# Optimization experiments

Hardware: AMD Instinct MI355X
Metric: run time of the kernel (lower is better)

Reference implementation:

```python
import jax, jax.numpy as jnp
import numpy as np
from jax import lax

BN_EPS = 1e-5

def _conv(x, w, groups=1, pad=0):
    return lax.conv_general_dilated(
        x, w, window_strides=(1, 1), padding=[(pad, pad), (pad, pad)],
        dimension_numbers=('NCHW', 'OIHW', 'NCHW'), feature_group_count=groups)

def _gather2d(imgf, yi, xi, H, W):
    # imgf: [B,C,H*W] flattened image; yi, xi: [B,C,H,W] int32 corner indices
    valid = (yi >= 0) & (yi < H) & (xi >= 0) & (xi < W)
    yc = jnp.clip(yi, 0, H - 1)
    xc = jnp.clip(xi, 0, W - 1)
    idx = (yc * W + xc).reshape(imgf.shape[0], imgf.shape[1], -1)
    v = jnp.take_along_axis(imgf, idx, axis=2).reshape(yi.shape)
    return jnp.where(valid, v, 0.0)

def _bilinear_sample(img, y, x):
    # img: [B,C,H,W]; y, x: [B,C,H,W] float sample coords (zero outside)
    B, C, H, W = img.shape
    imgf = img.reshape(B, C, H * W)
    y0 = jnp.floor(y)
    x0 = jnp.floor(x)
    wy = y - y0  # weight for y1 corner
    wx = x - x0
    y0i = y0.astype(jnp.int32); y1i = y0i + 1
    x0i = x0.astype(jnp.int32); x1i = x0i + 1
    v00 = _gather2d(imgf, y0i, x0i, H, W)
    v01 = _gather2d(imgf, y0i, x1i, H, W)
    v10 = _gather2d(imgf, y1i, x0i, H, W)
    v11 = _gather2d(imgf, y1i, x1i, H, W)
    return ((1 - wy) * (1 - wx) * v00 + (1 - wy) * wx * v01
            + wy * (1 - wx) * v10 + wy * wx * v11)

def setup_inputs() -> dict:
    key = jax.random.key(0)
    ks = jax.random.split(key, 6)
    B, C, OC, H, W = 4, 64, 64, 256, 256
    return {
        'x': jax.random.normal(ks[0], (B, C, H, W), jnp.float32),
        'dw_weight': jax.random.normal(ks[1], (C, 1, 3, 3), jnp.float32) * 0.2,
        'pw_weight': jax.random.normal(ks[2], (3 * C, C, 1, 1), jnp.float32) * 0.1,
        'weight': jax.random.normal(ks[3], (OC, C, 1, 1), jnp.float32) * 0.1,
        'bias': jax.random.normal(ks[4], (OC,), jnp.float32) * 0.1,
        'gamma': jnp.ones((OC,), jnp.float32),
        'beta': jnp.zeros((OC,), jnp.float32),
    }

def reference(x, dw_weight, pw_weight, weight, bias, gamma, beta):
    B, C, H, W = x.shape
    # DWConv2d: depthwise 3x3 (pad 1) then pointwise 1x1 -> 3C channels
    om = _conv(_conv(x, dw_weight, groups=C, pad=1), pw_weight)
    offset_y = om[:, :C]
    offset_x = om[:, C:2 * C]
    modulator = 2.0 * jax.nn.sigmoid(om[:, 2 * C:])
    max_off = max(H, W) // 4
    offset = jnp.clip(jnp.concatenate([offset_y, offset_x], axis=1), -max_off, max_off)
    # torchvision deform_conv2d layout: [B, og*2, H, W] interleaved (y, x) per offset group
    off = offset.reshape(B, C, 2, H, W)
    hh = jnp.arange(H, dtype=x.dtype)[:, None]
    ww = jnp.arange(W, dtype=x.dtype)[None, :]
    sy = hh + off[:, :, 0]  # [B,C,H,W]
    sx = ww + off[:, :, 1]
    sampled = _bilinear_sample(x, sy, sx) * modulator
    w2 = weight.reshape(weight.shape[0], C)  # 1x1 kernel -> [OC, C]
    out = jnp.einsum('oc,bchw->bohw', w2, sampled) + bias[None, :, None, None]
    # BatchNorm2d (training-mode batch stats) + exact GELU
    mean = out.mean(axis=(0, 2, 3), keepdims=True)
    var = out.var(axis=(0, 2, 3), keepdims=True)
    out = (out - mean) * lax.rsqrt(var + BN_EPS)
    out = out * gamma[None, :, None, None] + beta[None, :, None, None]
    return jax.nn.gelu(out, approximate=False)
```

## Files before the change

kernel.cpp:

```cpp
#include <hip/hip_runtime.h>

#define B_  4
#define C_  64
#define H_  256
#define W_  256
#define HW_ 65536
#define NPIX_ (B_*HW_)
#define NELEM_ (B_*C_*HW_)

#define OMS 200
#define TS  72

typedef __attribute__((ext_vector_type(8))) short short8;
typedef __attribute__((ext_vector_type(4))) float floatx4;

static __device__ __forceinline__ unsigned short f2bf(float f){
  unsigned u = __float_as_uint(f);
  u += 0x7fff + ((u >> 16) & 1);
  return (unsigned short)(u >> 16);
}
static __device__ __forceinline__ float bf2f(unsigned short s){
  return __uint_as_float(((unsigned)s) << 16);
}
static __device__ __forceinline__ unsigned pack2(float a, float b){
  return (unsigned)f2bf(a) | ((unsigned)f2bf(b) << 16);
}

__global__ __launch_bounds__(256) void k_cvtw(
    const float* __restrict__ pw, const float* __restrict__ w2,
    unsigned short* __restrict__ wB)
{
  int i = blockIdx.x*256 + threadIdx.x;
  wB[i] = f2bf(i < 12288 ? pw[i] : w2[i - 12288]);
}

__global__ __launch_bounds__(256) void k_cvtx(
    const float4* __restrict__ X4, uint2* __restrict__ Y)
{
  int i = blockIdx.x*256 + threadIdx.x;
  float4 a = X4[i];
  uint2 u; u.x = pack2(a.x, a.y); u.y = pack2(a.z, a.w);
  Y[i] = u;
}

__global__ __launch_bounds__(256) void k_dwconv(
    const unsigned short* __restrict__ xB,
    const float* __restrict__ dwW,
    unsigned short* __restrict__ t)
{
  int tid = threadIdx.x;
  int bid = ((blockIdx.x & 7) << 9) + (blockIdx.x >> 3);
  int b    = bid >> 10;
  int tile = bid & 1023;
  int h    = tile >> 2;
  int w0   = (tile & 3) << 6;
  int p  = tid & 63;
  int cg = tid >> 6;
  int wg = w0 + p;

  unsigned pk[8];
#pragma unroll
  for (int i = 0; i < 16; ++i){
    int c = cg*16 + i;
    const unsigned short* xp = xB + ((size_t)(b*C_ + c) << 16);
    const float* wp = dwW + c*9;
    float acc = 0.f;
#pragma unroll
    for (int dy = -1; dy <= 1; ++dy){
      int hy = h + dy;
      if ((unsigned)hy >= (unsigned)H_) continue;
      const unsigned short* row = xp + (hy << 8);
#pragma unroll
      for (int dx = -1; dx <= 1; ++dx){
        int wx = wg + dx;
        if ((unsigned)wx >= (unsigned)W_) continue;
        acc += wp[(dy+1)*3 + (dx+1)] * bf2f(row[wx]);
      }
    }
    unsigned short bv = f2bf(acc);
    if (i & 1) pk[i>>1] |= ((unsigned)bv << 16);
    else       pk[i>>1]  = (unsigned)bv;
  }
  size_t rowbase = ((size_t)bid*64 + p)*64 + cg*16;
  uint4 u0; u0.x = pk[0]; u0.y = pk[1]; u0.z = pk[2]; u0.w = pk[3];
  uint4 u1; u1.x = pk[4]; u1.y = pk[5]; u1.z = pk[6]; u1.w = pk[7];
  *(uint4*)(t + rowbase)     = u0;
  *(uint4*)(t + rowbase + 8) = u1;
}

__global__ __launch_bounds__(256, 5) void k_fuse(
    const unsigned short* __restrict__ xB,
    const unsigned short* __restrict__ t,
    const unsigned short* __restrict__ pwB,
    const unsigned short* __restrict__ w2B,
    unsigned short* __restrict__ outB,
    float* __restrict__ gsumS,
    float* __restrict__ gsqS)
{
  __shared__ __align__(16) char lds[25600];
  unsigned short* OM = (unsigned short*)lds;
  unsigned short* T  = (unsigned short*)lds;
  float* red1 = (float*)(lds + 9216);
  float* red2 = (float*)(lds + 10240);

  int tid = threadIdx.x;
  int bid = ((blockIdx.x & 7) << 9) + (blockIdx.x >> 3);
  int wv = tid >> 6, lane = tid & 63;
  int mrow = lane & 15, q = lane >> 4;
  int px0 = bid*64;
  int pxw = px0 + wv*16;

  short8 bfrag[2];
#pragma unroll
  for (int kb = 0; kb < 2; ++kb)
    bfrag[kb] = *(const short8*)(t + (size_t)(pxw + mrow)*64 + kb*32 + q*8);

  floatx4 acc[12];
#pragma unroll
  for (int mt = 0; mt < 12; ++mt) acc[mt] = (floatx4){0.f,0.f,0.f,0.f};
#pragma unroll
  for (int kb = 0; kb < 2; ++kb)
#pragma unroll
    for (int mt = 0; mt < 12; ++mt){
      short8 af = *(const short8*)(pwB + (mt*16 + mrow)*64 + kb*32 + q*8);
      acc[mt] = __builtin_amdgcn_mfma_f32_16x16x32_bf16(af, bfrag[kb], acc[mt], 0, 0, 0);
    }

  {
    int omrow = (wv*16 + mrow)*OMS;
#pragma unroll
    for (int mt = 0; mt < 12; ++mt){
      uint2 u; u.x = pack2(acc[mt][0], acc[mt][1]); u.y = pack2(acc[mt][2], acc[mt][3]);
      *(uint2*)(OM + omrow + mt*16 + q*4) = u;
    }
  }
  __syncthreads();

  unsigned pk[8];
  {
    int pl = tid >> 2;
    int cg = tid & 3;
    int px = px0 + pl;
    int b = px >> 16;
    int p = px & (HW_-1);
    int h = p >> 8, w = p & (W_-1);

    const char* xbyte = (const char*)(xB + ((size_t)(b*C_ + cg*16) << 16));
    float hf = (float)h, wf = (float)w;

    float rw0[8], rw1[8], cwA[8], cwB[8];
    unsigned pu0[8], pu1[8];

#pragma unroll
    for (int half = 0; half < 2; ++half){
      const uint4* ob = (const uint4*)(OM + pl*OMS + cg*32 + half*16);
      uint4 oA = ob[0], oB = ob[1];
      uint4 mv = *(const uint4*)(OM + pl*OMS + 128 + cg*16 + half*8);
      unsigned pr[8] = {oA.x,oA.y,oA.z,oA.w, oB.x,oB.y,oB.z,oB.w};
      unsigned md4[4] = {mv.x,mv.y,mv.z,mv.w};

#pragma unroll
      for (int i = 0; i < 8; ++i){
        unsigned pair = pr[i];
        float oy = __uint_as_float(pair << 16);
        float ox = __uint_as_float(pair & 0xffff0000u);
        float mm = __uint_as_float((i & 1) ? (md4[i>>1] & 0xffff0000u)
                                           : (md4[i>>1] << 16));
        float mod = 2.f / (1.f + __expf(-mm));
        oy = fminf(fmaxf(oy, -64.f), 64.f);
        ox = fminf(fmaxf(ox, -64.f), 64.f);
        float sy = hf + oy, sx = wf + ox;
        float y0f = floorf(sy), x0f = floorf(sx);
        float wy = sy - y0f, wxr = sx - x0f;
        int y0 = (int)y0f, x0 = (int)x0f;
        int yc0 = min(max(y0,     0), 255);
        int yc1 = min(max(y0 + 1, 0), 255);
        int xc  = min(max(x0, 0), 254);
        bool y0v = ((unsigned)y0       < 256u);
        bool y1v = ((unsigned)(y0 + 1) < 256u);
        bool x0v = ((unsigned)x0       < 256u);
        bool x1v = ((unsigned)(x0 + 1) < 256u);
        bool x0lo = (x0 == xc);
        float r0 = y0v ? (1.f - wy) * mod : 0.f;
        float r1 = y1v ? wy * mod : 0.f;
        float c0w = x0v ? (1.f - wxr) : 0.f;
        float c1w = x1v ? wxr : 0.f;
        rw0[i] = r0; rw1[i] = r1;
        cwA[i] = x0lo ? c0w : c1w;
        cwB[i] = x0lo ? c1w : c0w;
        unsigned cb  = ((unsigned)(half*8 + i)) << 17;
        unsigned o0  = cb + ((unsigned)yc0 << 9) + ((unsigned)xc << 1);
        unsigned o1  = cb + ((unsigned)yc1 << 9) + ((unsigned)xc << 1);
        __builtin_memcpy(&pu0[i], xbyte + o0, 4);
        __builtin_memcpy(&pu1[i], xbyte + o1, 4);
      }
#pragma unroll
      for (int i = 0; i < 8; ++i){
        int ci = half*8 + i;
        float lo0 = __uint_as_float(pu0[i] << 16);
        float hi0 = __uint_as_float(pu0[i] & 0xffff0000u);
        float lo1 = __uint_as_float(pu1[i] << 16);
        float hi1 = __uint_as_float(pu1[i] & 0xffff0000u);
        float sres = rw0[i] * (cwA[i]*lo0 + cwB[i]*hi0)
                   + rw1[i] * (cwA[i]*lo1 + cwB[i]*hi1);
        unsigned short bv = f2bf(sres);
        if (ci & 1) pk[ci>>1] |= ((unsigned)bv << 16);
        else        pk[ci>>1]  = (unsigned)bv;
      }
    }
  }
  __syncthreads();

  {
    int pl = tid >> 2, cg = tid & 3;
    uint4 u0; u0.x = pk[0]; u0.y = pk[1]; u0.z = pk[2]; u0.w = pk[3];
    uint4 u1; u1.x = pk[4]; u1.y = pk[5]; u1.z = pk[6]; u1.w = pk[7];
    *(uint4*)(T + pl*TS + cg*16)     = u0;
    *(uint4*)(T + pl*TS + cg*16 + 8) = u1;
  }
  __syncthreads();

  short8 a2[2];
#pragma unroll
  for (int kb = 0; kb < 2; ++kb)
    a2[kb] = *(const short8*)(T + (wv*16 + mrow)*TS + kb*32 + q*8);

  floatx4 acc2[4];
#pragma unroll
  for (int nt = 0; nt < 4; ++nt) acc2[nt] = (floatx4){0.f,0.f,0.f,0.f};
#pragma unroll
  for (int kb = 0; kb < 2; ++kb)
#pragma unroll
    for (int nt = 0; nt < 4; ++nt){
      short8 bf = *(const short8*)(w2B + (nt*16 + mrow)*64 + kb*32 + q*8);
      acc2[nt] = __builtin_amdgcn_mfma_f32_16x16x32_bf16(a2[kb], bf, acc2[nt], 0, 0, 0);
    }

  int b   = pxw >> 16;
  int hw0 = pxw & (HW_-1);
#pragma unroll
  for (int nt = 0; nt < 4; ++nt){
    int och = nt*16 + mrow;
    float a0 = acc2[nt][0], a1 = acc2[nt][1], a2v = acc2[nt][2], a3 = acc2[nt][3];
    uint2 u; u.x = pack2(a0, a1); u.y = pack2(a2v, a3);
    *(uint2*)(outB + ((size_t)(b*C_ + och) << 16) + hw0 + q*4) = u;
    float s1 = a0 + a1 + a2v + a3;
    float s2 = a0*a0 + a1*a1 + a2v*a2v + a3*a3;
    s1 += __shfl_xor(s1, 16, 64);  s2 += __shfl_xor(s2, 16, 64);
    s1 += __shfl_xor(s1, 32, 64);  s2 += __shfl_xor(s2, 32, 64);
    if (q == 0){ red1[wv*64 + och] = s1; red2[wv*64 + och] = s2; }
  }
  __syncthreads();
  if (tid < 64){
    float t1 = red1[tid] + red1[64+tid] + red1[128+tid] + red1[192+tid];
    float t2 = red2[tid] + red2[64+tid] + red2[128+tid] + red2[192+tid];
    int slot = blockIdx.x & 31;
    atomicAdd(&gsumS[slot*64 + tid], t1);
    atomicAdd(&gsqS[slot*64 + tid], t2);
  }
}

__global__ void k_finalize(const float* __restrict__ gsumS, const float* __restrict__ gsqS,
                           const float* __restrict__ gamma, const float* __restrict__ beta,
                           float* __restrict__ scale, float* __restrict__ shift)
{
  int o = threadIdx.x;
  if (o < 64){
    float s1 = 0.f, s2 = 0.f;
    for (int s = 0; s < 32; ++s){ s1 += gsumS[s*64 + o]; s2 += gsqS[s*64 + o]; }
    float n = (float)NPIX_;
    float mean = s1 / n;
    float var  = s2 / n - mean*mean;
    float sc = gamma[o] * rsqrtf(var + 1e-5f);
    scale[o] = sc;
    shift[o] = beta[o] - mean*sc;
  }
}

__global__ __launch_bounds__(256) void k_bn_gelu(
    const uint4* __restrict__ outB4,
    const float* __restrict__ scale,
    const float* __restrict__ shift,
    float4* __restrict__ y4)
{
  int i = blockIdx.x*256 + threadIdx.x;
  int och = (i >> 13) & 63;
  float sc = scale[och], sh = shift[och];
  uint4 u = outB4[i];
  float e[8];
  e[0] = bf2f((unsigned short)(u.x & 0xffffu)); e[1] = bf2f((unsigned short)(u.x >> 16));
  e[2] = bf2f((unsigned short)(u.y & 0xffffu)); e[3] = bf2f((unsigned short)(u.y >> 16));
  e[4] = bf2f((unsigned short)(u.z & 0xffffu)); e[5] = bf2f((unsigned short)(u.z >> 16));
  e[6] = bf2f((unsigned short)(u.w & 0xffffu)); e[7] = bf2f((unsigned short)(u.w >> 16));
  float4 o0, o1;
  float a;
  a = e[0]*sc + sh; o0.x = 0.5f*a*(1.f + erff(a*0.70710678118654752f));
  a = e[1]*sc + sh; o0.y = 0.5f*a*(1.f + erff(a*0.70710678118654752f));
  a = e[2]*sc + sh; o0.z = 0.5f*a*(1.f + erff(a*0.70710678118654752f));
  a = e[3]*sc + sh; o0.w = 0.5f*a*(1.f + erff(a*0.70710678118654752f));
  a = e[4]*sc + sh; o1.x = 0.5f*a*(1.f + erff(a*0.70710678118654752f));
  a = e[5]*sc + sh; o1.y = 0.5f*a*(1.f + erff(a*0.70710678118654752f));
  a = e[6]*sc + sh; o1.z = 0.5f*a*(1.f + erff(a*0.70710678118654752f));
  a = e[7]*sc + sh; o1.w = 0.5f*a*(1.f + erff(a*0.70710678118654752f));
  y4[2*i]   = o0;
  y4[2*i+1] = o1;
}

extern "C" void kernel_launch(void* const* d_in, const int* in_sizes, int n_in,
                              void* d_out, int out_size, void* d_ws, size_t ws_size,
                              hipStream_t stream)
{
  (void)in_sizes; (void)n_in; (void)out_size; (void)ws_size;
  const float* x     = (const float*)d_in[0];
  const float* dw    = (const float*)d_in[1];
  const float* pw    = (const float*)d_in[2];
  const float* w2    = (const float*)d_in[3];
  const float* gamma = (const float*)d_in[5];
  const float* beta  = (const float*)d_in[6];

  char* ws = (char*)d_ws;
  unsigned short* xB    = (unsigned short*)ws;
  unsigned short* t     = (unsigned short*)(ws + 33554432);
  unsigned short* outB  = (unsigned short*)(ws + 67108864);
  float*          stats = (float*)(ws + 100663296);
  float* gsumS = stats;
  float* gsqS  = stats + 2048;
  float* scale = stats + 4096;
  float* shift = stats + 4160;
  unsigned short* wB  = (unsigned short*)(ws + 100680192);
  unsigned short* pwB = wB;
  unsigned short* w2B = wB + 12288;

  k_cvtw    <<<64, 256, 0, stream>>>(pw, w2, wB);
  k_cvtx    <<<NELEM_/4/256, 256, 0, stream>>>((const float4*)x, (uint2*)xB);
  hipMemsetAsync(stats, 0, 16384, stream);
  k_dwconv  <<<NPIX_/64, 256, 0, stream>>>(xB, dw, t);
  k_fuse    <<<NPIX_/64, 256, 0, stream>>>(xB, t, pwB, w2B, outB, gsumS, gsqS);
  k_finalize<<<1, 64, 0, stream>>>(gsumS, gsqS, gamma, beta, scale, shift);
  k_bn_gelu <<<NELEM_/8/256, 256, 0, stream>>>((const uint4*)outB, scale, shift,
                                               (float4*)d_out);
}
```

Before: 320.4 us.

## Fuse fp32-to-bf16 input conversion into depthwise conv and remap sampling threads

```diff
diff --git a/kernel.cpp b/kernel.cpp
--- a/kernel.cpp
+++ b/kernel.cpp
@@ -34,18 +34,10 @@
   wB[i] = f2bf(i < 12288 ? pw[i] : w2[i - 12288]);
 }
 
-__global__ __launch_bounds__(256) void k_cvtx(
-    const float4* __restrict__ X4, uint2* __restrict__ Y)
-{
-  int i = blockIdx.x*256 + threadIdx.x;
-  float4 a = X4[i];
-  uint2 u; u.x = pack2(a.x, a.y); u.y = pack2(a.z, a.w);
-  Y[i] = u;
-}
-
 __global__ __launch_bounds__(256) void k_dwconv(
-    const unsigned short* __restrict__ xB,
+    const float* __restrict__ x,
     const float* __restrict__ dwW,
+    unsigned short* __restrict__ xB,
     unsigned short* __restrict__ t)
 {
   int tid = threadIdx.x;
@@ -62,21 +54,25 @@
 #pragma unroll
   for (int i = 0; i < 16; ++i){
     int c = cg*16 + i;
-    const unsigned short* xp = xB + ((size_t)(b*C_ + c) << 16);
+    const float* xp = x + ((size_t)(b*C_ + c) << 16);
     const float* wp = dwW + c*9;
     float acc = 0.f;
+    float ctr = 0.f;
 #pragma unroll
     for (int dy = -1; dy <= 1; ++dy){
       int hy = h + dy;
       if ((unsigned)hy >= (unsigned)H_) continue;
-      const unsigned short* row = xp + (hy << 8);
+      const float* row = xp + (hy << 8);
 #pragma unroll
       for (int dx = -1; dx <= 1; ++dx){
         int wx = wg + dx;
         if ((unsigned)wx >= (unsigned)W_) continue;
-        acc += wp[(dy+1)*3 + (dx+1)] * bf2f(row[wx]);
+        float v = row[wx];
+        if (dy == 0 && dx == 0) ctr = v;
+        acc += wp[(dy+1)*3 + (dx+1)] * v;
       }
     }
+    xB[((size_t)(b*C_ + c) << 16) + (h << 8) + wg] = f2bf(ctr);
     unsigned short bv = f2bf(acc);
     if (i & 1) pk[i>>1] |= ((unsigned)bv << 16);
     else       pk[i>>1]  = (unsigned)bv;
@@ -138,8 +134,8 @@
 
   unsigned pk[8];
   {
-    int pl = tid >> 2;
-    int cg = tid & 3;
+    int pl = tid & 63;
+    int cg = tid >> 6;
     int px = px0 + pl;
     int b = px >> 16;
     int p = px & (HW_-1);
@@ -212,7 +208,7 @@
   __syncthreads();
 
   {
-    int pl = tid >> 2, cg = tid & 3;
+    int pl = tid & 63, cg = tid >> 6;
     uint4 u0; u0.x = pk[0]; u0.y = pk[1]; u0.z = pk[2]; u0.w = pk[3];
     uint4 u1; u1.x = pk[4]; u1.y = pk[5]; u1.z = pk[6]; u1.w = pk[7];
     *(uint4*)(T + pl*TS + cg*16)     = u0;
@@ -332,9 +328,8 @@
   unsigned short* w2B = wB + 12288;
 
   k_cvtw    <<<64, 256, 0, stream>>>(pw, w2, wB);
-  k_cvtx    <<<NELEM_/4/256, 256, 0, stream>>>((const float4*)x, (uint2*)xB);
   hipMemsetAsync(stats, 0, 16384, stream);
-  k_dwconv  <<<NPIX_/64, 256, 0, stream>>>(xB, dw, t);
+  k_dwconv  <<<NPIX_/64, 256, 0, stream>>>(x, dw, xB, t);
   k_fuse    <<<NPIX_/64, 256, 0, stream>>>(xB, t, pwB, w2B, outB, gsumS, gsqS);
   k_finalize<<<1, 64, 0, stream>>>(gsumS, gsqS, gamma, beta, scale, shift);
   k_bn_gelu <<<NELEM_/8/256, 256, 0, stream>>>((const uint4*)outB, scale, shift,
```

Result: no change. 325.1 us (+1.5%).
